# Kernel tuning notes

Measured on AMD Instinct MI355X. Metric: run time of the kernel, lower is better.

The kernel has to match this reference:

```python
import jax, jax.numpy as jnp
import numpy as np


def setup_inputs() -> dict:
    key = jax.random.key(0)
    k_cb, k_mask, k_y, k_yt, k_ym = jax.random.split(key, 5)
    B, L, M = 8, 2048, 4096
    CB = jax.random.normal(k_cb, (B, L, 3), dtype=jnp.float32) * 10.0
    # residue validity mask: mostly valid, some padding
    mask = (jax.random.uniform(k_mask, (B, L)) > 0.1).astype(jnp.float32)
    Y = jax.random.normal(k_y, (B, M, 3), dtype=jnp.float32) * 10.0
    Y_t = jax.random.randint(k_yt, (B, M), 0, 64, dtype=jnp.int32)
    Y_m = jax.random.randint(k_ym, (B, M), 0, 2, dtype=jnp.int32)
    return {"CB": CB, "mask": mask, "Y": Y, "Y_t": Y_t, "Y_m": Y_m,
            "number_of_ligand_atoms": 25}


def reference(CB, mask, Y, Y_t, Y_m, number_of_ligand_atoms):
    # CB: [B, L, 3], mask: [B, L], Y: [B, M, 3], Y_t/Y_m: [B, M]
    B, L, _ = CB.shape
    k = number_of_ligand_atoms
    Y_m_f = Y_m.astype(jnp.float32)
    mask_CBY = mask[:, :, None] * Y_m_f[:, None, :]          # [B, L, M]
    d = CB[:, :, None, :] - Y[:, None, :, :]                 # [B, L, M, 3]
    L2_AB = jnp.sum(d * d, axis=-1)                          # [B, L, M]
    L2_AB = L2_AB * mask_CBY + (1.0 - mask_CBY) * 1000.0
    # k smallest distances per (b, l); torch uses full argsort + slice,
    # top_k of the negated matrix selects the same set.
    neg_vals, nn_idx = jax.lax.top_k(-L2_AB, k)              # [B, L, k]
    L2_AB_nn = -neg_vals
    D_AB_closest = jnp.sqrt(L2_AB_nn[:, :, 0])               # [B, L]
    b_idx = jnp.arange(B)[:, None, None]                     # [B, 1, 1]
    Y_out = Y[b_idx, nn_idx]                                 # [B, L, k, 3]
    Y_t_out = Y_t[b_idx, nn_idx].astype(jnp.int32)           # [B, L, k]
    Y_m_out = Y_m[b_idx, nn_idx].astype(jnp.int32)           # [B, L, k]
    return Y_out, Y_t_out, Y_m_out, D_AB_closest
```

## Files before the change

kernel.cpp:

```cpp
#include <hip/hip_runtime.h>

#pragma clang fp contract(off)

typedef unsigned long long u64;
typedef unsigned int u32;

#define BB 8
#define LL 2048
#define MM 4096
#define KK 25
#define WPB 16
#define TPB 1024
#define CAP 3072
#define SENT 0xFFFFFFFFFFFFFFFFull

static __device__ __forceinline__ u32 wave_min_u32(u32 x) {
    u32 t;
    t = (u32)__builtin_amdgcn_update_dpp(0, (int)x, 0xB1, 0xF, 0xF, true);
    x = t < x ? t : x;
    t = (u32)__builtin_amdgcn_update_dpp(0, (int)x, 0x4E, 0xF, 0xF, true);
    x = t < x ? t : x;
    t = (u32)__builtin_amdgcn_update_dpp(0, (int)x, 0x141, 0xF, 0xF, true);
    x = t < x ? t : x;
    t = (u32)__builtin_amdgcn_update_dpp(0, (int)x, 0x140, 0xF, 0xF, true);
    x = t < x ? t : x;
    t = (u32)__builtin_amdgcn_update_dpp((int)x, (int)x, 0x142, 0xF, 0xF, false);
    x = t < x ? t : x;
    t = (u32)__builtin_amdgcn_update_dpp((int)x, (int)x, 0x143, 0xF, 0xF, false);
    x = t < x ? t : x;
    return (u32)__builtin_amdgcn_readlane((int)x, 63);
}

__global__ void __launch_bounds__(TPB, 8) knn_kernel(
    const float* __restrict__ CB, const float* __restrict__ maskA,
    const float* __restrict__ Y, const int* __restrict__ Yt,
    const int* __restrict__ Ym, float* __restrict__ out)
{
    __shared__ float4 sC[CAP];
    __shared__ unsigned short sMidx[64];
    __shared__ int sWinc[16];
    __shared__ int sWbase[16];
    __shared__ int sVtot;
    __shared__ u64 sWin[WPB][KK];

    const int tid  = threadIdx.x;
    const int lane = tid & 63;
    const int wv   = tid >> 6;
    const int blk  = blockIdx.x;
    const int b    = blk >> 7;
    const int qg   = blk & 127;

    const float* Yb  = Y  + (size_t)b * MM * 3;
    const int*   Ymb = Ym + (size_t)b * MM;
    const int*   Ytb = Yt + (size_t)b * MM;

    const int p0 = tid << 2;
    const float4 f0 = *(const float4*)(Yb + 3 * p0);
    const float4 f1 = *(const float4*)(Yb + 3 * p0 + 4);
    const float4 f2 = *(const float4*)(Yb + 3 * p0 + 8);
    const int4   m4 = *(const int4*)(Ymb + p0);
    const int v0 = (m4.x != 0), v1 = (m4.y != 0), v2 = (m4.z != 0), v3 = (m4.w != 0);
    const int cnt = v0 + v1 + v2 + v3;

    int inc = cnt;
#pragma unroll
    for (int off = 1; off < 64; off <<= 1) {
        const int t = __shfl_up(inc, off, 64);
        if (lane >= off) inc += t;
    }
    if (lane == 63) sWinc[wv] = inc;
    __syncthreads();
    if (tid < 16) {
        const int x = sWinc[tid];
        int ix = x;
#pragma unroll
        for (int off = 1; off < 16; off <<= 1) {
            const int t = __shfl_up(ix, off, 16);
            if (tid >= off) ix += t;
        }
        sWbase[tid] = ix - x;
        if (tid == 15) sVtot = ix;
    }
    __syncthreads();

    {
        int bs = sWbase[wv] + inc - cnt;
        int mb = p0 - bs;
        if (v0) { sC[bs++] = make_float4(f0.x, f0.y, f0.z, (float)(p0 + 0)); }
        else    { if (mb < 64) sMidx[mb] = (unsigned short)(p0 + 0); mb++; }
        if (v1) { sC[bs++] = make_float4(f0.w, f1.x, f1.y, (float)(p0 + 1)); }
        else    { if (mb < 64) sMidx[mb] = (unsigned short)(p0 + 1); mb++; }
        if (v2) { sC[bs++] = make_float4(f1.z, f1.w, f2.x, (float)(p0 + 2)); }
        else    { if (mb < 64) sMidx[mb] = (unsigned short)(p0 + 2); mb++; }
        if (v3) { sC[bs++] = make_float4(f2.y, f2.z, f2.w, (float)(p0 + 3)); }
        else    { if (mb < 64) sMidx[mb] = (unsigned short)(p0 + 3); mb++; }
    }
    const int V  = sVtot;
    const int NJ = (V + 63) >> 6;
    for (int c = V + tid; c < (NJ << 6); c += TPB)
        sC[c] = make_float4(__builtin_inff(), 0.0f, 0.0f, 4095.0f);
    __syncthreads();

    const int l = qg * WPB + wv;
    const int q = b * LL + l;

    float* out_y = out;
    float* out_t = out + (size_t)BB * LL * KK * 3;
    float* out_m = out_t + (size_t)BB * LL * KK;
    float* out_d = out_m + (size_t)BB * LL * KK;

    if (maskA[q] == 0.0f) {
        if (lane < KK) {
            const int p = lane;
            const size_t o = (size_t)q * KK + lane;
            out_y[3 * o + 0] = Yb[3 * p + 0];
            out_y[3 * o + 1] = Yb[3 * p + 1];
            out_y[3 * o + 2] = Yb[3 * p + 2];
            out_t[o] = (float)Ytb[p];
            out_m[o] = (float)Ymb[p];
            if (lane == 0) out_d[q] = sqrtf(1000.0f);
        }
        return;
    }

    const float cx = CB[3 * q + 0];
    const float cy = CB[3 * q + 1];
    const float cz = CB[3 * q + 2];

    float v1f = 3.0e38f, v2f = 3.0e38f, v3f = 3.0e38f, v4f = 3.0e38f;
    u32 J = 0u;
    const u32 SEL1 = 0x06050400u;
    const u32 SEL2 = 0x06050004u;
    const u32 SEL3 = 0x06000504u;
    const u32 SEL4 = 0x00060504u;
#pragma unroll 4
    for (int j = 0; j < NJ; ++j) {
        const float4 c = sC[(j << 6) | lane];
        const float dx = cx - c.x;
        const float dy = cy - c.y;
        const float dz = cz - c.z;
        const float v = (dx * dx + dy * dy) + dz * dz;
        const bool c1 = v < v1f, c2 = v < v2f, c3 = v < v3f, c4 = v < v4f;
        const u32 sel = c1 ? SEL1 : (c2 ? SEL2 : (c3 ? SEL3 : SEL4));
        const u32 Jp  = __builtin_amdgcn_perm(J, (u32)j, sel);
        const float n2 = __builtin_amdgcn_fmed3f(v, v1f, v2f);
        const float n3 = __builtin_amdgcn_fmed3f(v, v2f, v3f);
        const float n4 = __builtin_amdgcn_fmed3f(v, v3f, v4f);
        v1f = fminf(v, v1f);
        v2f = n2; v3f = n3; v4f = n4;
        J = c4 ? Jp : J;
    }

    const float* sCw = (const float*)sC;
    const u32 p1 = (u32)sCw[((((J      ) & 0xFFu) << 6) | lane) * 4 + 3];
    const u32 p2 = (u32)sCw[((((J >>  8) & 0xFFu) << 6) | lane) * 4 + 3];
    const u32 p3 = (u32)sCw[((((J >> 16) & 0xFFu) << 6) | lane) * 4 + 3];
    const u32 p4 = (u32)sCw[((((J >> 24) & 0xFFu) << 6) | lane) * 4 + 3];

    u64 k1 = ((u64)(__float_as_uint(v1f) + 1u) << 32) | p1;
    u64 k2 = ((u64)(__float_as_uint(v2f) + 1u) << 32) | p2;
    u64 k3 = ((u64)(__float_as_uint(v3f) + 1u) << 32) | p3;
    u64 k4 = ((u64)(__float_as_uint(v4f) + 1u) << 32) | p4;
    u64 lref = k4;

#pragma unroll 1
    for (int it = 0; it < KK; ++it) {
        const bool need = (k1 == SENT);
        if (__any(need)) {
            u64 found = SENT;
#pragma unroll 4
            for (int j = 0; j < NJ; ++j) {
                const float4 c = sC[(j << 6) | lane];
                const float dx = cx - c.x;
                const float dy = cy - c.y;
                const float dz = cz - c.z;
                const float v = (dx * dx + dy * dy) + dz * dz;
                const u64 key = ((u64)(__float_as_uint(v) + 1u) << 32)
                              | (u32)c.w;
                if (key > lref && key < found) found = key;
            }
            if (need) { k1 = found; lref = found; }
        }
        const u32 vh = (u32)(k1 >> 32);
        const u32 bv = wave_min_u32(vh);
        const u64 ball = __ballot(vh == bv);
        bool win = (vh == bv);
        if (__popcll(ball) != 1) {
            const u32 vl = (u32)k1;
            u32 cp = win ? vl : 0xFFFFFFFFu;
#pragma unroll
            for (int off = 32; off; off >>= 1) {
                const u32 o = __shfl_xor(cp, off, 64);
                cp = (o < cp) ? o : cp;
            }
            win = win && (vl == cp);
        }
        if (win) {
            sWin[wv][it] = k1;
            k1 = k2; k2 = k3; k3 = k4; k4 = SENT;
        }
    }

    u64 mykey = 0;
    if (lane < KK) mykey = sWin[wv][lane];
    const u32 mvh = (u32)(mykey >> 32);
    const bool less = (lane < KK) && (mvh < 0x447A0001u);
    const int nless = __popcll(__ballot(less));
    if (lane < KK) {
        int p; float val, mflag;
        if (lane < nless) {
            p = (int)(u32)mykey;
            val = __uint_as_float(mvh - 1u);
            mflag = 1.0f;
        } else {
            p = (int)sMidx[lane - nless];
            val = 1000.0f;
            mflag = 0.0f;
        }
        const size_t o = (size_t)q * KK + lane;
        out_y[3 * o + 0] = Yb[3 * p + 0];
        out_y[3 * o + 1] = Yb[3 * p + 1];
        out_y[3 * o + 2] = Yb[3 * p + 2];
        out_t[o] = (float)Ytb[p];
        out_m[o] = mflag;
        if (lane == 0) out_d[q] = sqrtf(val);
    }
}

extern "C" void kernel_launch(void* const* d_in, const int* in_sizes, int n_in,
                              void* d_out, int out_size, void* d_ws, size_t ws_size,
                              hipStream_t stream) {
    const float* CB   = (const float*)d_in[0];
    const float* mask = (const float*)d_in[1];
    const float* Y    = (const float*)d_in[2];
    const int*   Yt   = (const int*)d_in[3];
    const int*   Ym   = (const int*)d_in[4];
    float* out = (float*)d_out;

    dim3 grid(BB * LL / WPB);
    dim3 block(TPB);
    hipLaunchKernelGGL(knn_kernel, grid, block, 0, stream, CB, mask, Y, Yt, Ym, out);
}
```

Baseline: 102.9 us.

## Store candidates as SoA in LDS and process two per lane with packed math

```diff
diff --git a/kernel.cpp b/kernel.cpp
--- a/kernel.cpp
+++ b/kernel.cpp
@@ -4,6 +4,8 @@
 
 typedef unsigned long long u64;
 typedef unsigned int u32;
+typedef unsigned short u16;
+typedef float f32x2 __attribute__((ext_vector_type(2)));
 
 #define BB 8
 #define LL 2048
@@ -36,8 +38,11 @@
     const float* __restrict__ Y, const int* __restrict__ Yt,
     const int* __restrict__ Ym, float* __restrict__ out)
 {
-    __shared__ float4 sC[CAP];
-    __shared__ unsigned short sMidx[64];
+    __shared__ __align__(16) float sX[CAP];
+    __shared__ __align__(16) float sY[CAP];
+    __shared__ __align__(16) float sZ[CAP];
+    __shared__ u16 sP16[CAP];
+    __shared__ u16 sMidx[64];
     __shared__ int sWinc[16];
     __shared__ int sWbase[16];
     __shared__ int sVtot;
@@ -86,19 +91,20 @@
     {
         int bs = sWbase[wv] + inc - cnt;
         int mb = p0 - bs;
-        if (v0) { sC[bs++] = make_float4(f0.x, f0.y, f0.z, (float)(p0 + 0)); }
-        else    { if (mb < 64) sMidx[mb] = (unsigned short)(p0 + 0); mb++; }
-        if (v1) { sC[bs++] = make_float4(f0.w, f1.x, f1.y, (float)(p0 + 1)); }
-        else    { if (mb < 64) sMidx[mb] = (unsigned short)(p0 + 1); mb++; }
-        if (v2) { sC[bs++] = make_float4(f1.z, f1.w, f2.x, (float)(p0 + 2)); }
-        else    { if (mb < 64) sMidx[mb] = (unsigned short)(p0 + 2); mb++; }
-        if (v3) { sC[bs++] = make_float4(f2.y, f2.z, f2.w, (float)(p0 + 3)); }
-        else    { if (mb < 64) sMidx[mb] = (unsigned short)(p0 + 3); mb++; }
+        if (v0) { sX[bs]=f0.x; sY[bs]=f0.y; sZ[bs]=f0.z; sP16[bs]=(u16)(p0+0); bs++; }
+        else    { if (mb < 64) sMidx[mb] = (u16)(p0 + 0); mb++; }
+        if (v1) { sX[bs]=f0.w; sY[bs]=f1.x; sZ[bs]=f1.y; sP16[bs]=(u16)(p0+1); bs++; }
+        else    { if (mb < 64) sMidx[mb] = (u16)(p0 + 1); mb++; }
+        if (v2) { sX[bs]=f1.z; sY[bs]=f1.w; sZ[bs]=f2.x; sP16[bs]=(u16)(p0+2); bs++; }
+        else    { if (mb < 64) sMidx[mb] = (u16)(p0 + 2); mb++; }
+        if (v3) { sX[bs]=f2.y; sY[bs]=f2.z; sZ[bs]=f2.w; sP16[bs]=(u16)(p0+3); bs++; }
+        else    { if (mb < 64) sMidx[mb] = (u16)(p0 + 3); mb++; }
     }
     const int V  = sVtot;
-    const int NJ = (V + 63) >> 6;
-    for (int c = V + tid; c < (NJ << 6); c += TPB)
-        sC[c] = make_float4(__builtin_inff(), 0.0f, 0.0f, 4095.0f);
+    const int NJ = (V + 127) >> 7;
+    for (int c = V + tid; c < (NJ << 7); c += TPB) {
+        sX[c] = __builtin_inff(); sY[c] = 0.0f; sZ[c] = 0.0f; sP16[c] = 4095;
+    }
     __syncthreads();
 
     const int l = qg * WPB + wv;
@@ -133,34 +139,41 @@
     const u32 SEL2 = 0x06050004u;
     const u32 SEL3 = 0x06000504u;
     const u32 SEL4 = 0x00060504u;
-#pragma unroll 4
-    for (int j = 0; j < NJ; ++j) {
-        const float4 c = sC[(j << 6) | lane];
-        const float dx = cx - c.x;
-        const float dy = cy - c.y;
-        const float dz = cz - c.z;
-        const float v = (dx * dx + dy * dy) + dz * dz;
+    auto ins = [&](float v, u32 id) {
         const bool c1 = v < v1f, c2 = v < v2f, c3 = v < v3f, c4 = v < v4f;
         const u32 sel = c1 ? SEL1 : (c2 ? SEL2 : (c3 ? SEL3 : SEL4));
-        const u32 Jp  = __builtin_amdgcn_perm(J, (u32)j, sel);
+        const u32 Jp  = __builtin_amdgcn_perm(J, id, sel);
         const float n2 = __builtin_amdgcn_fmed3f(v, v1f, v2f);
         const float n3 = __builtin_amdgcn_fmed3f(v, v2f, v3f);
         const float n4 = __builtin_amdgcn_fmed3f(v, v3f, v4f);
         v1f = fminf(v, v1f);
         v2f = n2; v3f = n3; v4f = n4;
         J = c4 ? Jp : J;
-    }
-
-    const float* sCw = (const float*)sC;
-    const u32 p1 = (u32)sCw[((((J      ) & 0xFFu) << 6) | lane) * 4 + 3];
-    const u32 p2 = (u32)sCw[((((J >>  8) & 0xFFu) << 6) | lane) * 4 + 3];
-    const u32 p3 = (u32)sCw[((((J >> 16) & 0xFFu) << 6) | lane) * 4 + 3];
-    const u32 p4 = (u32)sCw[((((J >> 24) & 0xFFu) << 6) | lane) * 4 + 3];
-
-    u64 k1 = ((u64)(__float_as_uint(v1f) + 1u) << 32) | p1;
-    u64 k2 = ((u64)(__float_as_uint(v2f) + 1u) << 32) | p2;
-    u64 k3 = ((u64)(__float_as_uint(v3f) + 1u) << 32) | p3;
-    u64 k4 = ((u64)(__float_as_uint(v4f) + 1u) << 32) | p4;
+    };
+
+    const f32x2 cxx = {cx, cx}, cyy = {cy, cy}, czz = {cz, cz};
+#pragma unroll 2
+    for (int j = 0; j < NJ; ++j) {
+        const int base = (j << 7) + (lane << 1);
+        const f32x2 xp = *(const f32x2*)&sX[base];
+        const f32x2 yp = *(const f32x2*)&sY[base];
+        const f32x2 zp = *(const f32x2*)&sZ[base];
+        const f32x2 dx = cxx - xp;
+        const f32x2 dy = cyy - yp;
+        const f32x2 dz = czz - zp;
+        const f32x2 dsq = (dx * dx + dy * dy) + dz * dz;
+        ins(dsq.x, (u32)(j << 1));
+        ins(dsq.y, (u32)((j << 1) | 1));
+    }
+
+    auto slotof = [&](u32 id) -> u32 {
+        return ((id >> 1) << 7) | (u32)(lane << 1) | (id & 1u);
+    };
+
+    u64 k1 = ((u64)(__float_as_uint(v1f) + 1u) << 32) | slotof( J        & 0xFFu);
+    u64 k2 = ((u64)(__float_as_uint(v2f) + 1u) << 32) | slotof((J >>  8) & 0xFFu);
+    u64 k3 = ((u64)(__float_as_uint(v3f) + 1u) << 32) | slotof((J >> 16) & 0xFFu);
+    u64 k4 = ((u64)(__float_as_uint(v4f) + 1u) << 32) | slotof((J >> 24) & 0xFFu);
     u64 lref = k4;
 
 #pragma unroll 1
@@ -168,15 +181,15 @@
         const bool need = (k1 == SENT);
         if (__any(need)) {
             u64 found = SENT;
+            const int NI = NJ << 1;
 #pragma unroll 4
-            for (int j = 0; j < NJ; ++j) {
-                const float4 c = sC[(j << 6) | lane];
-                const float dx = cx - c.x;
-                const float dy = cy - c.y;
-                const float dz = cz - c.z;
+            for (int id = 0; id < NI; ++id) {
+                const u32 s = slotof((u32)id);
+                const float dx = cx - sX[s];
+                const float dy = cy - sY[s];
+                const float dz = cz - sZ[s];
                 const float v = (dx * dx + dy * dy) + dz * dz;
-                const u64 key = ((u64)(__float_as_uint(v) + 1u) << 32)
-                              | (u32)c.w;
+                const u64 key = ((u64)(__float_as_uint(v) + 1u) << 32) | s;
                 if (key > lref && key < found) found = key;
             }
             if (need) { k1 = found; lref = found; }
@@ -209,7 +222,7 @@
     if (lane < KK) {
         int p; float val, mflag;
         if (lane < nless) {
-            p = (int)(u32)mykey;
+            p = (int)sP16[(u32)mykey & 0xFFFFu];
             val = __uint_as_float(mvh - 1u);
             mflag = 1.0f;
         } else {
```

Measured after the change: 104.1 us. Within noise of the previous version (+1.1%).
